# Kernel optimization log

Hardware: AMD Instinct MI355X
Metric: run time of the kernel (lower is better)

## Reference

```python
import jax, jax.numpy as jnp
import numpy as np


def setup_inputs() -> dict:
    key = jax.random.key(0)
    k1, k2 = jax.random.split(key)
    mat_1 = jax.random.normal(k1, (100000, 64), dtype=jnp.float32)
    mat_2 = jax.random.normal(k2, (2048, 64), dtype=jnp.float32)
    return {"mat_1": mat_1, "mat_2": mat_2}


def reference(mat_1, mat_2):
    # Squared euclidean distance between every row of mat_1 and mat_2.
    # Same math as sum((a - b)**2) = ||a||^2 + ||b||^2 - 2 a.b,
    # expressed as a single GEMM plus broadcast adds.
    sq1 = jnp.sum(mat_1 * mat_1, axis=1, keepdims=True)        # (n_1, 1)
    sq2 = jnp.sum(mat_2 * mat_2, axis=1)                       # (n_2,)
    cross = jnp.einsum('nd,md->nm', mat_1, mat_2)              # (n_1, n_2)
    dist = sq1 + sq2[None, :] - 2.0 * cross
    return dist
```

## Files before the change

kernel.cpp:

```cpp
#include <hip/hip_runtime.h>
#include <cstdint>
#include <cstddef>


typedef __bf16 v8bf __attribute__((ext_vector_type(8)));
typedef float  v4f  __attribute__((ext_vector_type(4)));

__device__ inline unsigned short f32_to_bf16_rne(float f) {
    union { float f; uint32_t u; } c; c.f = f;
    uint32_t u = c.u;
    uint32_t r = (u + 0x7fffu + ((u >> 16) & 1u)) >> 16;
    return (unsigned short)r;
}

__global__ __launch_bounds__(256) void prep_kernel(const float* __restrict__ B,
                                                   unsigned short* __restrict__ Bbf,
                                                   float* __restrict__ sq2, int N) {
    int t = blockIdx.x * 256 + threadIdx.x;
    int row = t >> 2;
    if (row >= N) return;
    int q = (t & 3) * 16;
    const float* src = B + (size_t)row * 64 + q;
    unsigned short* dst = Bbf + (size_t)row * 64 + q;
    float s = 0.f;
#pragma unroll
    for (int i = 0; i < 4; ++i) {
        float4 v = *reinterpret_cast<const float4*>(src + 4 * i);
        s += v.x * v.x + v.y * v.y + v.z * v.z + v.w * v.w;
        uint2 p;
        p.x = (uint32_t)f32_to_bf16_rne(-2.f * v.x) | ((uint32_t)f32_to_bf16_rne(-2.f * v.y) << 16);
        p.y = (uint32_t)f32_to_bf16_rne(-2.f * v.z) | ((uint32_t)f32_to_bf16_rne(-2.f * v.w) << 16);
        *reinterpret_cast<uint2*>(dst + 4 * i) = p;
    }
    s += __shfl_xor(s, 1);
    s += __shfl_xor(s, 2);
    if ((t & 3) == 0) sq2[row] = s;
}

__global__ __launch_bounds__(512, 1) void dist_kernel(const float* __restrict__ A,
                                                      const unsigned short* __restrict__ Bbf,
                                                      const float* __restrict__ sq2,
                                                      float* __restrict__ out,
                                                      int M, int N, int NT) {
    __shared__ __align__(16) unsigned char b_lds[131072];

    const int t = threadIdx.x;
    const int h = blockIdx.x >> 8;
    const int s = blockIdx.x & 255;
    const int NH = N >> 1;

    {
        const unsigned short* src = Bbf + (size_t)h * NH * 64;
        const int nchunk = NH * 8;
        for (int idx = t; idx < nchunk; idx += 512) {
            int col = idx >> 3, q = idx & 7;
            uint4 v = *reinterpret_cast<const uint4*>(src + col * 64 + q * 8);
            int L = col * 128 + q * 16;
            *reinterpret_cast<uint4*>(b_lds + (L ^ ((col & 7) << 4))) = v;
        }
    }
    __syncthreads();

    const int lane = t & 63;
    const int w    = t >> 6;
    const int lg   = lane >> 4;
    const int li   = lane & 15;
    const int swz  = (li & 7) << 4;

    v4f s2v[2][4];
#pragma unroll
    for (int cc = 0; cc < 2; ++cc)
#pragma unroll
        for (int ct = 0; ct < 4; ++ct)
            s2v[cc][ct] = *reinterpret_cast<const v4f*>(
                &sq2[h * NH + cc * 512 + w * 64 + 16 * ct + 4 * lg]);

    v8bf bf[2][4][2];
#pragma unroll
    for (int cc = 0; cc < 2; ++cc)
#pragma unroll
        for (int ct = 0; ct < 4; ++ct)
#pragma unroll
            for (int kb = 0; kb < 2; ++kb) {
                int col = cc * 512 + w * 64 + 16 * ct + li;
                int L = col * 128 + kb * 64 + lg * 16;
                bf[cc][ct][kb] = *reinterpret_cast<const v8bf*>(b_lds + (L ^ swz));
            }

    for (int tt = s; tt < NT; tt += 256) {
        const int m0 = tt * 64;
        const bool full = (m0 + 64 <= M);

        v8bf  af[4][2];
        float s1[4];
#pragma unroll
        for (int rt = 0; rt < 4; ++rt) {
            int r = m0 + 16 * rt + li; if (r >= M) r = M - 1;
            const float* ar = A + (size_t)r * 64;
            float ss = 0.f;
#pragma unroll
            for (int kb = 0; kb < 2; ++kb) {
                float4 x0 = *reinterpret_cast<const float4*>(ar + kb * 32 + 8 * lg);
                float4 x1 = *reinterpret_cast<const float4*>(ar + kb * 32 + 8 * lg + 4);
                ss += x0.x * x0.x + x0.y * x0.y + x0.z * x0.z + x0.w * x0.w;
                ss += x1.x * x1.x + x1.y * x1.y + x1.z * x1.z + x1.w * x1.w;
                union { v8bf v; unsigned short u[8]; } pk;
                pk.u[0] = f32_to_bf16_rne(x0.x); pk.u[1] = f32_to_bf16_rne(x0.y);
                pk.u[2] = f32_to_bf16_rne(x0.z); pk.u[3] = f32_to_bf16_rne(x0.w);
                pk.u[4] = f32_to_bf16_rne(x1.x); pk.u[5] = f32_to_bf16_rne(x1.y);
                pk.u[6] = f32_to_bf16_rne(x1.z); pk.u[7] = f32_to_bf16_rne(x1.w);
                af[rt][kb] = pk.v;
            }
            ss += __shfl_xor(ss, 16);
            ss += __shfl_xor(ss, 32);
            s1[rt] = ss;
        }

#pragma unroll
        for (int cc = 0; cc < 2; ++cc) {
            v4f acc[4][4];
#pragma unroll
            for (int rt = 0; rt < 4; ++rt)
#pragma unroll
                for (int ct = 0; ct < 4; ++ct)
                    acc[rt][ct] = s2v[cc][ct] + s1[rt];

#pragma unroll
            for (int rt = 0; rt < 4; ++rt)
#pragma unroll
                for (int ct = 0; ct < 4; ++ct) {
                    acc[rt][ct] = __builtin_amdgcn_mfma_f32_16x16x32_bf16(bf[cc][ct][0], af[rt][0], acc[rt][ct], 0, 0, 0);
                    acc[rt][ct] = __builtin_amdgcn_mfma_f32_16x16x32_bf16(bf[cc][ct][1], af[rt][1], acc[rt][ct], 0, 0, 0);
                }

            const int cbase = h * NH + cc * 512 + w * 64;
            if (full) {
#pragma unroll
                for (int rt = 0; rt < 4; ++rt) {
                    float* orow = out + (size_t)(m0 + 16 * rt + li) * N + cbase;
#pragma unroll
                    for (int ct = 0; ct < 4; ++ct)
                        *reinterpret_cast<v4f*>(orow + 16 * ct + 4 * lg) = acc[rt][ct];
                }
            } else {
#pragma unroll
                for (int rt = 0; rt < 4; ++rt) {
                    int r = m0 + 16 * rt + li;
                    if (r < M) {
                        float* orow = out + (size_t)r * N + cbase;
#pragma unroll
                        for (int ct = 0; ct < 4; ++ct)
                            *reinterpret_cast<v4f*>(orow + 16 * ct + 4 * lg) = acc[rt][ct];
                    }
                }
            }
        }
    }
}

extern "C" void kernel_launch(void* const* d_in, const int* in_sizes, int n_in,
                              void* d_out, int out_size, void* d_ws, size_t ws_size,
                              hipStream_t stream) {
    const float* A = (const float*)d_in[0];
    const float* B = (const float*)d_in[1];
    const int M = in_sizes[0] / 64;
    const int N = in_sizes[1] / 64;

    unsigned short* Bbf = (unsigned short*)d_ws;
    float* sq2 = (float*)((char*)d_ws + (size_t)N * 64 * sizeof(unsigned short));
    float* out = (float*)d_out;

    prep_kernel<<<(N * 4 + 255) / 256, 256, 0, stream>>>(B, Bbf, sq2, N);

    const int NT = (M + 63) / 64;
    dist_kernel<<<512, 512, 0, stream>>>(A, Bbf, sq2, out, M, N, NT);
}
```

Baseline: 200.6 us.

## Stage output through LDS for coalesced nontemporal stores and prefetch next A tile

Row tiles shrink from 64 to 32 rows, and the next tile of A is loaded into registers while the current tile is computed, hiding load latency. Output accumulators go through a per-wave swizzled LDS stage so each 8-lane group writes a contiguous 128-byte row segment. Those writes use nontemporal stores, which targets the write-bandwidth-bound output of about 800MB. It costs extra LDS traffic and loop overhead per tile, and within-wave LDS reuse without explicit barriers depends on wave-synchronous execution.

```diff
diff --git a/kernel.cpp b/kernel.cpp
--- a/kernel.cpp
+++ b/kernel.cpp
@@ -43,6 +43,7 @@
                                                       float* __restrict__ out,
                                                       int M, int N, int NT) {
     __shared__ __align__(16) unsigned char b_lds[131072];
+    __shared__ __align__(16) float stage_lds[8][512];
 
     const int t = threadIdx.x;
     const int h = blockIdx.x >> 8;
@@ -66,6 +67,7 @@
     const int lg   = lane >> 4;
     const int li   = lane & 15;
     const int swz  = (li & 7) << 4;
+    float* const stg = &stage_lds[w][0];
 
     v4f s2v[2][4];
 #pragma unroll
@@ -87,21 +89,36 @@
                 bf[cc][ct][kb] = *reinterpret_cast<const v8bf*>(b_lds + (L ^ swz));
             }
 
-    for (int tt = s; tt < NT; tt += 256) {
-        const int m0 = tt * 64;
-        const bool full = (m0 + 64 <= M);
-
-        v8bf  af[4][2];
-        float s1[4];
-#pragma unroll
-        for (int rt = 0; rt < 4; ++rt) {
+    float4 raw[8];
+    auto loadA = [&](int tt) {
+        const int m0 = tt * 32;
+#pragma unroll
+        for (int rt = 0; rt < 2; ++rt) {
             int r = m0 + 16 * rt + li; if (r >= M) r = M - 1;
             const float* ar = A + (size_t)r * 64;
+#pragma unroll
+            for (int kb = 0; kb < 2; ++kb) {
+                raw[rt * 4 + kb * 2]     = *reinterpret_cast<const float4*>(ar + kb * 32 + 8 * lg);
+                raw[rt * 4 + kb * 2 + 1] = *reinterpret_cast<const float4*>(ar + kb * 32 + 8 * lg + 4);
+            }
+        }
+    };
+
+    loadA(s);
+
+#pragma unroll 1
+    for (int tt = s; tt < NT; tt += 256) {
+        const int m0 = tt * 32;
+
+        v8bf  af[2][2];
+        float s1[2];
+#pragma unroll
+        for (int rt = 0; rt < 2; ++rt) {
             float ss = 0.f;
 #pragma unroll
             for (int kb = 0; kb < 2; ++kb) {
-                float4 x0 = *reinterpret_cast<const float4*>(ar + kb * 32 + 8 * lg);
-                float4 x1 = *reinterpret_cast<const float4*>(ar + kb * 32 + 8 * lg + 4);
+                float4 x0 = raw[rt * 4 + kb * 2];
+                float4 x1 = raw[rt * 4 + kb * 2 + 1];
                 ss += x0.x * x0.x + x0.y * x0.y + x0.z * x0.z + x0.w * x0.w;
                 ss += x1.x * x1.x + x1.y * x1.y + x1.z * x1.z + x1.w * x1.w;
                 union { v8bf v; unsigned short u[8]; } pk;
@@ -116,17 +133,22 @@
             s1[rt] = ss;
         }
 
+        {
+            int tn = tt + 256; if (tn >= NT) tn = tt;
+            loadA(tn);
+        }
+
 #pragma unroll
         for (int cc = 0; cc < 2; ++cc) {
-            v4f acc[4][4];
-#pragma unroll
-            for (int rt = 0; rt < 4; ++rt)
+            v4f acc[2][4];
+#pragma unroll
+            for (int rt = 0; rt < 2; ++rt)
 #pragma unroll
                 for (int ct = 0; ct < 4; ++ct)
                     acc[rt][ct] = s2v[cc][ct] + s1[rt];
 
 #pragma unroll
-            for (int rt = 0; rt < 4; ++rt)
+            for (int rt = 0; rt < 2; ++rt)
 #pragma unroll
                 for (int ct = 0; ct < 4; ++ct) {
                     acc[rt][ct] = __builtin_amdgcn_mfma_f32_16x16x32_bf16(bf[cc][ct][0], af[rt][0], acc[rt][ct], 0, 0, 0);
@@ -134,23 +156,26 @@
                 }
 
             const int cbase = h * NH + cc * 512 + w * 64;
-            if (full) {
-#pragma unroll
-                for (int rt = 0; rt < 4; ++rt) {
-                    float* orow = out + (size_t)(m0 + 16 * rt + li) * N + cbase;
-#pragma unroll
-                    for (int ct = 0; ct < 4; ++ct)
-                        *reinterpret_cast<v4f*>(orow + 16 * ct + 4 * lg) = acc[rt][ct];
-                }
-            } else {
-#pragma unroll
-                for (int rt = 0; rt < 4; ++rt) {
-                    int r = m0 + 16 * rt + li;
-                    if (r < M) {
-                        float* orow = out + (size_t)r * N + cbase;
-#pragma unroll
-                        for (int ct = 0; ct < 4; ++ct)
-                            *reinterpret_cast<v4f*>(orow + 16 * ct + 4 * lg) = acc[rt][ct];
+#pragma unroll
+            for (int rt = 0; rt < 2; ++rt) {
+#pragma unroll
+                for (int hf = 0; hf < 2; ++hf) {
+#pragma unroll
+                    for (int q = 0; q < 2; ++q) {
+                        int c = 16 * q + 4 * lg;
+                        *reinterpret_cast<v4f*>(&stg[li * 32 + (c ^ (4 * (li & 7)))]) =
+                            acc[rt][2 * hf + q];
+                    }
+#pragma unroll
+                    for (int g = 0; g < 2; ++g) {
+                        int r2 = 8 * g + (lane >> 3);
+                        int c2 = 4 * (lane & 7);
+                        v4f v = *reinterpret_cast<const v4f*>(
+                            &stg[r2 * 32 + (c2 ^ (4 * (r2 & 7)))]);
+                        int grow = m0 + 16 * rt + r2;
+                        if (grow < M)
+                            __builtin_nontemporal_store(v,
+                                reinterpret_cast<v4f*>(out + (size_t)grow * N + cbase + 32 * hf + c2));
                     }
                 }
             }
@@ -172,6 +197,6 @@
 
     prep_kernel<<<(N * 4 + 255) / 256, 256, 0, stream>>>(B, Bbf, sq2, N);
 
-    const int NT = (M + 63) / 64;
+    const int NT = (M + 31) / 32;
     dist_kernel<<<512, 512, 0, stream>>>(A, Bbf, sq2, out, M, N, NT);
 }
```

Result: faster. 164.6 us (-17.9%).
